# Kernel optimization log

Measured on AMD Instinct MI355X. Metric: run time of the kernel, lower is better.

Reference implementation:

```python
import jax, jax.numpy as jnp
import numpy as np

N_NODES = 50000
N_EDGES = 600000
D = 128
LN_EPS = 1e-5


def setup_inputs() -> dict:
    key = jax.random.key(0)
    ks = jax.random.split(key, 10)
    s = 1.0 / np.sqrt(D)
    return {
        "node_reps": jax.random.normal(ks[0], (N_NODES, D), jnp.float32),
        "edge_reps": jax.random.normal(ks[1], (N_EDGES, D), jnp.float32),
        "src_idx": jax.random.randint(ks[2], (N_EDGES,), 0, N_NODES, jnp.int32),
        "dst_idx": jnp.sort(jax.random.randint(ks[3], (N_EDGES,), 0, N_NODES, jnp.int32)),
        "Wq": jax.random.normal(ks[4], (D, D), jnp.float32) * s,
        "Wk": jax.random.normal(ks[5], (D, D), jnp.float32) * s,
        "Wv": jax.random.normal(ks[6], (D, D), jnp.float32) * s,
        "Wo": jax.random.normal(ks[7], (D, D), jnp.float32) * s,
        "ln_gamma": jnp.ones((D,), jnp.float32),
        "ln_beta": jnp.zeros((D,), jnp.float32),
        "W1": jax.random.normal(ks[8], (3 * D, D), jnp.float32) * (1.0 / np.sqrt(3 * D)),
        "b1": jnp.zeros((D,), jnp.float32),
        "W2": jax.random.normal(ks[9], (D, D), jnp.float32) * s,
        "b2": jnp.zeros((D,), jnp.float32),
    }


def _layer_norm(x, g, b):
    mu = jnp.mean(x, axis=-1, keepdims=True)
    var = jnp.mean(jnp.square(x - mu), axis=-1, keepdims=True)
    return (x - mu) * jax.lax.rsqrt(var + LN_EPS) * g + b


def reference(node_reps, edge_reps, src_idx, dst_idx, Wq, Wk, Wv, Wo,
              ln_gamma, ln_beta, W1, b1, W2, b2):
    n_nodes, d = node_reps.shape
    # dense projections once per node (kernel-friendly GEMMs)
    q = node_reps @ Wq                                  # [N, d]
    k_nodes = node_reps @ Wk                            # [N, d]
    v_nodes = node_reps @ Wv                            # [N, d]
    # per-edge gather + edge bias
    k_e = k_nodes[src_idx] + edge_reps                  # [E, d]
    scores = jnp.sum(q[dst_idx] * k_e, axis=-1) / jnp.sqrt(jnp.float32(d))  # [E]
    # segment softmax over edges sharing the same dst node
    seg_max = jax.ops.segment_max(scores, dst_idx, num_segments=n_nodes)
    ex = jnp.exp(scores - seg_max[dst_idx])
    denom = jax.ops.segment_sum(ex, dst_idx, num_segments=n_nodes)
    alpha = ex / denom[dst_idx]                          # [E]
    v_e = v_nodes[src_idx] + edge_reps                   # [E, d]
    agg = jax.ops.segment_sum(alpha[:, None] * v_e, dst_idx, num_segments=n_nodes)  # [N, d]
    updated = _layer_norm(node_reps + agg @ Wo, ln_gamma, ln_beta)  # [N, d]
    # triplet fusion MLP over (dst node, edge, src node)
    h_trip = jnp.concatenate([node_reps[dst_idx], edge_reps, node_reps[src_idx]], axis=-1)  # [E, 3d]
    fused = jax.nn.relu(h_trip @ W1 + b1) @ W2 + b2      # [E, d]
    return updated, fused
```

## Files before the change

kernel.cpp:

```cpp
#include <hip/hip_runtime.h>
#include <hip/hip_bf16.h>

#define NN 50000
#define NE 600000
#define D 128

typedef __bf16 bf16x8 __attribute__((ext_vector_type(8)));
typedef __bf16 bf16x4 __attribute__((ext_vector_type(4)));
typedef float f32x4 __attribute__((ext_vector_type(4)));


static __device__ __forceinline__ bf16x8 load_a_frag_nc(const float* __restrict__ A,
                                                        int row, int k0) {
  const f32x4* p = (const f32x4*)(A + (size_t)row * D + k0);
  f32x4 v0 = p[0], v1 = p[1];
  bf16x8 r;
  r[0] = (__bf16)v0[0]; r[1] = (__bf16)v0[1]; r[2] = (__bf16)v0[2]; r[3] = (__bf16)v0[3];
  r[4] = (__bf16)v1[0]; r[5] = (__bf16)v1[1]; r[6] = (__bf16)v1[2]; r[7] = (__bf16)v1[3];
  return r;
}

static __device__ __forceinline__ void stage_a_tile128(const float* __restrict__ A, int M,
                                                       int row_base, char* lds, int tid) {
  const int l32 = tid & 31;
  const int g = tid >> 5;
#pragma unroll
  for (int it = 0; it < 16; ++it) {
    int rl = it * 8 + g;
    int r = row_base + rl;
    f32x4 v = {};
    if (r < M) v = *(const f32x4*)(A + (size_t)r * D + l32 * 4);
    bf16x4 b;
    b[0] = (__bf16)v[0]; b[1] = (__bf16)v[1]; b[2] = (__bf16)v[2]; b[3] = (__bf16)v[3];
    int byte = (rl * 256 + l32 * 8) ^ ((rl & 7) << 4);
    *(bf16x4*)(lds + byte) = b;
  }
}

static __device__ __forceinline__ bf16x8 read_a_frag(const char* lds, int rl, int k0) {
  int byte = (rl * 256 + k0 * 2) ^ ((rl & 7) << 4);
  return *(const bf16x8*)(lds + byte);
}

template <int CTRL>
static __device__ __forceinline__ float dpp_add(float x) {
  int v = __builtin_amdgcn_update_dpp(0, __float_as_int(x), CTRL, 0xf, 0xf, true);
  return x + __int_as_float(v);
}

static __device__ __forceinline__ float red32(float x) {
  x = dpp_add<0xB1>(x);
  x = dpp_add<0x4E>(x);
  x = dpp_add<0x124>(x);
  x = dpp_add<0x128>(x);
  return x + __shfl_xor(x, 16, 64);
}

#define CATT 0.12751744612764933f

struct PrepArgs {
  const float* W[8];
  __bf16* WT[8];
  const int* dst;
  int* offs;
};

__global__ void prep_all(PrepArgs pa) {
  int b = blockIdx.x;
  if (b < 512) {
    int w = b >> 6;
    int t = (b & 63) * 256 + threadIdx.x;
    int n = t & 127, k = t >> 7;
    float v = pa.W[w][k * 128 + n];
    if (w == 0) v *= CATT;
    pa.WT[w][n * 128 + k] = (__bf16)v;
  } else {
    int n = (b - 512) * 256 + threadIdx.x;
    if (n > NN) return;
    int lo = 0, hi = NE;
    while (lo < hi) {
      int mid = (lo + hi) >> 1;
      if (pa.dst[mid] < n) lo = mid + 1; else hi = mid;
    }
    pa.offs[n] = lo;
  }
}

struct GemmBatch {
  const __bf16* BT[5];
  void* C[5];
  const float* bias[5];
  int mode[5];
};

__global__ __launch_bounds__(256) void gemm_k128_b(const float* __restrict__ A,
                                                   GemmBatch gb, int M) {
  __shared__ __align__(16) char atile[128 * 256];
  const int y = blockIdx.y;
  const __bf16* __restrict__ BT = gb.BT[y];
  const int tid = threadIdx.x;
  const int lane = tid & 63;
  const int wave = tid >> 6;
  const int wr = wave >> 1, wc = wave & 1;
  const int row0 = blockIdx.x * 128;
  const int col0 = wc * 64;
  const int lr = lane & 15;
  const int lk = (lane >> 4) << 3;

  stage_a_tile128(A, M, row0, atile, tid);
  __syncthreads();

  f32x4 acc[4][4] = {};
#pragma unroll
  for (int kk = 0; kk < 4; ++kk) {
    const int k0 = kk * 32 + lk;
    bf16x8 a[4], b[4];
#pragma unroll
    for (int m = 0; m < 4; ++m) a[m] = read_a_frag(atile, wr * 64 + m * 16 + lr, k0);
#pragma unroll
    for (int n = 0; n < 4; ++n) b[n] = *(const bf16x8*)(BT + (size_t)(col0 + n * 16 + lr) * D + k0);
#pragma unroll
    for (int m = 0; m < 4; ++m)
#pragma unroll
      for (int n = 0; n < 4; ++n)
        acc[m][n] = __builtin_amdgcn_mfma_f32_16x16x32_bf16(a[m], b[n], acc[m][n], 0, 0, 0);
  }
  const int rr = (lane >> 4) * 4;
  float bv[4] = {0.f, 0.f, 0.f, 0.f};
  if (gb.bias[y]) {
#pragma unroll
    for (int n = 0; n < 4; ++n) bv[n] = gb.bias[y][col0 + n * 16 + lr];
  }
  const int mode = gb.mode[y];
#pragma unroll
  for (int m = 0; m < 4; ++m)
#pragma unroll
    for (int j = 0; j < 4; ++j) {
      const int row = row0 + wr * 64 + m * 16 + rr + j;
      if (row < M) {
#pragma unroll
        for (int n = 0; n < 4; ++n) {
          const int c = col0 + n * 16 + lr;
          const float val = acc[m][n][j] + bv[n];
          if (mode == 0) {
            ((float*)gb.C[y])[(size_t)row * D + c] = val;
          } else if (mode == 1) {
            ((__bf16*)gb.C[y])[(size_t)row * D + c] = (__bf16)val;
          } else {
            const int e = ((c >> 2) << 3) + (c & 3) + (mode == 3 ? 4 : 0);
            ((__bf16*)gb.C[y])[(size_t)row * 256 + e] = (__bf16)val;
          }
        }
      }
    }
}

#define LD1(P, K, J, SV)                                                     \
  do {                                                                       \
    const int jj_ = (J);                                                     \
    const int jc_ = jj_ < jm ? jj_ : 0;                                      \
    int si_ = __shfl((SV), jj_ & 31, 32);                                    \
    si_ = jj_ < jm ? si_ : 0;                                                \
    kv##P[K] = *(const bf16x8*)(KV + (size_t)si_ * 256 + (l32 << 3));        \
    ee##P[K] = *(const f32x4*)(edge + (size_t)(s0 + jc_) * D + (l32 << 2));  \
  } while (0)

#define LOADC(P, C)                                                          \
  do {                                                                       \
    const int c4_ = (C) * 4;                                                 \
    const int sv_ = (c4_ < 32) ? sidx0 : sidx1;                              \
    LD1(P, 0, c4_ + 0, sv_); LD1(P, 1, c4_ + 1, sv_);                        \
    LD1(P, 2, c4_ + 2, sv_); LD1(P, 3, c4_ + 3, sv_);                        \
  } while (0)

#define CP1(P, K, J)                                                         \
  do {                                                                       \
    const int jj_ = (J);                                                     \
    f32x4 ef_ = ee##P[K];                                                    \
    float x0_ = (float)kv##P[K][0] + ef_[0];                                 \
    float x1_ = (float)kv##P[K][1] + ef_[1];                                 \
    float x2_ = (float)kv##P[K][2] + ef_[2];                                 \
    float x3_ = (float)kv##P[K][3] + ef_[3];                                 \
    float pp_ = fmaf(qs[1], x1_, qs[0] * x0_) + fmaf(qs[3], x3_, qs[2] * x2_); \
    float s_ = red32(pp_);                                                   \
    float w_ = jj_ < jm ? exp2f(s_) : 0.f;                                   \
    l += w_;                                                                 \
    a[0] = fmaf(w_, (float)kv##P[K][4] + ef_[0], a[0]);                      \
    a[1] = fmaf(w_, (float)kv##P[K][5] + ef_[1], a[1]);                      \
    a[2] = fmaf(w_, (float)kv##P[K][6] + ef_[2], a[2]);                      \
    a[3] = fmaf(w_, (float)kv##P[K][7] + ef_[3], a[3]);                      \
  } while (0)

#define COMPC(P, C)                                                          \
  do {                                                                       \
    const int cc4_ = (C) * 4;                                                \
    CP1(P, 0, cc4_ + 0); CP1(P, 1, cc4_ + 1);                                \
    CP1(P, 2, cc4_ + 2); CP1(P, 3, cc4_ + 3);                                \
  } while (0)

#define MEMFENCE asm volatile("" ::: "memory")

__global__ __launch_bounds__(256) __attribute__((amdgpu_waves_per_eu(4)))
void fused_edge_attn(
    const float* __restrict__ edge,
    const __bf16* __restrict__ W1bT,
    const __bf16* __restrict__ W2T,
    const __bf16* __restrict__ P1,
    const __bf16* __restrict__ P3,
    const int* __restrict__ dst,
    const int* __restrict__ src,
    const float* __restrict__ b2,
    float* __restrict__ out_fused,
    const float* __restrict__ Q,
    const __bf16* __restrict__ KV,
    const int* __restrict__ offs,
    const __bf16* __restrict__ WoT,
    const float* __restrict__ noderep,
    const float* __restrict__ gamma,
    const float* __restrict__ beta,
    float* __restrict__ out_updated) {
  __shared__ __align__(16) char buf[64 * 256];
  const int tid = threadIdx.x;
  const int b = blockIdx.x;
  const int x = b & 7;
  const int t = b >> 3;
  const int grp = (t / 5) * 8 + x;
  const int role = t % 5;
  if (grp >= 3125) return;

  if (role >= 2) {
    const int ebi = grp * 3 + (role - 2);
    const int eb = ebi * 64;
    const int lane = tid & 63;
    const int wave = tid >> 6;
    const int wr = wave >> 1, wc = wave & 1;
    const int lr = lane & 15;
    const int lk = (lane >> 4) << 3;
    const int col0 = wc * 64;
    const int rr = (lane >> 4) * 4;

    f32x4 acc[2][4] = {};
#pragma unroll
    for (int kk = 0; kk < 4; ++kk) {
      const int k0 = kk * 32 + lk;
      bf16x8 a[2], bm[4];
#pragma unroll
      for (int m = 0; m < 2; ++m) a[m] = load_a_frag_nc(edge, eb + wr * 32 + m * 16 + lr, k0);
#pragma unroll
      for (int n = 0; n < 4; ++n) bm[n] = *(const bf16x8*)(W1bT + (size_t)(col0 + n * 16 + lr) * D + k0);
#pragma unroll
      for (int m = 0; m < 2; ++m)
#pragma unroll
        for (int n = 0; n < 4; ++n)
          acc[m][n] = __builtin_amdgcn_mfma_f32_16x16x32_bf16(a[m], bm[n], acc[m][n], 0, 0, 0);
    }

#pragma unroll
    for (int m = 0; m < 2; ++m) {
#pragma unroll
      for (int j = 0; j < 4; ++j) {
        const int rl = wr * 32 + m * 16 + rr + j;
        const __bf16* __restrict__ p1r = P1 + (size_t)dst[eb + rl] * D;
        const __bf16* __restrict__ p3r = P3 + (size_t)src[eb + rl] * D;
#pragma unroll
        for (int n = 0; n < 4; ++n) {
          const int c = col0 + n * 16 + lr;
          float v = fmaxf(acc[m][n][j] + (float)p1r[c] + (float)p3r[c], 0.f);
          int byte = (rl * 256 + c * 2) ^ ((rl & 7) << 4);
          *(__bf16*)(buf + byte) = (__bf16)v;
        }
      }
    }
    __syncthreads();

    float b2v[4];
#pragma unroll
    for (int n = 0; n < 4; ++n) b2v[n] = b2[col0 + n * 16 + lr];
    f32x4 acc2[2][4] = {};
#pragma unroll
    for (int kk = 0; kk < 4; ++kk) {
      const int k0 = kk * 32 + lk;
      bf16x8 a[2], bm[4];
#pragma unroll
      for (int m = 0; m < 2; ++m) a[m] = read_a_frag(buf, wr * 32 + m * 16 + lr, k0);
#pragma unroll
      for (int n = 0; n < 4; ++n) bm[n] = *(const bf16x8*)(W2T + (size_t)(col0 + n * 16 + lr) * D + k0);
#pragma unroll
      for (int m = 0; m < 2; ++m)
#pragma unroll
        for (int n = 0; n < 4; ++n)
          acc2[m][n] = __builtin_amdgcn_mfma_f32_16x16x32_bf16(a[m], bm[n], acc2[m][n], 0, 0, 0);
    }
#pragma unroll
    for (int m = 0; m < 2; ++m)
#pragma unroll
      for (int j = 0; j < 4; ++j) {
        int rl = wr * 32 + m * 16 + rr + j;
        int e = eb + rl;
#pragma unroll
        for (int n = 0; n < 4; ++n) {
          int c = col0 + n * 16 + lr;
          out_fused[(size_t)e * D + c] = acc2[m][n][j] + b2v[n];
        }
      }
  } else {
    const int nw = tid >> 5;
    const int node = (grp * 2 + role) * 8 + nw;
    const int l32 = tid & 31;
    int s0 = offs[node], s1 = offs[node + 1];
    int cnt = s1 - s0;
    f32x4 qs = *(const f32x4*)(Q + (size_t)node * D + l32 * 4);
    float l = 0.f;
    f32x4 a = {0.f, 0.f, 0.f, 0.f};

    const int jm = cnt < 64 ? cnt : 64;
    if (jm > 0) {
      int sidx0 = 0, sidx1 = 0;
      if (l32 < cnt) sidx0 = src[s0 + l32];
      if (l32 + 32 < cnt) sidx1 = src[s0 + 32 + l32];
      bf16x8 kv0[4], kv1[4];
      f32x4 ee0[4], ee1[4];
      const int nch = (jm + 3) >> 2;
      LOADC(0, 0);
      MEMFENCE;
      for (int c = 0; c < nch; c += 2) {
        if (c + 1 < nch) LOADC(1, c + 1);
        MEMFENCE;
        COMPC(0, c);
        if (c + 2 < nch) LOADC(0, c + 2);
        MEMFENCE;
        if (c + 1 < nch) COMPC(1, c + 1);
      }
      for (int i = 64; i < cnt; ++i) {
        int si = src[s0 + i];
        bf16x8 kvx = *(const bf16x8*)(KV + (size_t)si * 256 + (l32 << 3));
        f32x4 ef = *(const f32x4*)(edge + (size_t)(s0 + i) * D + (l32 << 2));
        float x0 = (float)kvx[0] + ef[0], x1 = (float)kvx[1] + ef[1];
        float x2 = (float)kvx[2] + ef[2], x3 = (float)kvx[3] + ef[3];
        float pp = fmaf(qs[1], x1, qs[0] * x0) + fmaf(qs[3], x3, qs[2] * x2);
        float w = exp2f(red32(pp));
        l += w;
        a[0] = fmaf(w, (float)kvx[4] + ef[0], a[0]);
        a[1] = fmaf(w, (float)kvx[5] + ef[1], a[1]);
        a[2] = fmaf(w, (float)kvx[6] + ef[2], a[2]);
        a[3] = fmaf(w, (float)kvx[7] + ef[3], a[3]);
      }
    }
    float inv = l > 0.f ? 1.f / l : 0.f;
    f32x4 r;
    r[0] = a[0] * inv; r[1] = a[1] * inv; r[2] = a[2] * inv; r[3] = a[3] * inv;

    {
      bf16x4 rb;
      rb[0] = (__bf16)r[0]; rb[1] = (__bf16)r[1];
      rb[2] = (__bf16)r[2]; rb[3] = (__bf16)r[3];
      int byte = (nw * 256 + l32 * 8) ^ ((nw & 7) << 4);
      *(bf16x4*)(buf + byte) = rb;
    }
    __syncthreads();

    {
      const int wave = tid >> 6;
      const int lane = tid & 63;
      const int lr = lane & 15;
      const int lk = (lane >> 4) << 3;
      f32x4 acc[2] = {};
#pragma unroll
      for (int kk = 0; kk < 4; ++kk) {
        int k0 = kk * 32 + lk;
        bf16x8 af = read_a_frag(buf, lr, k0);
#pragma unroll
        for (int tt = 0; tt < 2; ++tt) {
          int nn = wave * 2 + tt;
          bf16x8 bm = *(const bf16x8*)(WoT + (size_t)(nn * 16 + lr) * D + k0);
          acc[tt] = __builtin_amdgcn_mfma_f32_16x16x32_bf16(af, bm, acc[tt], 0, 0, 0);
        }
      }
      float* xl = (float*)(buf + 8192);
      const int rr = (lane >> 4) * 4;
      if (rr < 8) {
#pragma unroll
        for (int tt = 0; tt < 2; ++tt) {
          int nn = wave * 2 + tt;
#pragma unroll
          for (int j = 0; j < 4; ++j)
            xl[(rr + j) * 128 + nn * 16 + lr] = acc[tt][j];
        }
      }
    }
    __syncthreads();

    {
      const float* xl = (const float*)(buf + 8192);
      f32x4 xv = *(const f32x4*)(xl + nw * 128 + l32 * 4);
      f32x4 nv = *(const f32x4*)(noderep + (size_t)node * D + l32 * 4);
      float x0 = xv[0] + nv[0], x1 = xv[1] + nv[1];
      float x2 = xv[2] + nv[2], x3 = xv[3] + nv[3];
      float s = red32(x0 + x1 + x2 + x3);
      float mu = s * (1.f / 128.f);
      float d0 = x0 - mu, d1 = x1 - mu, d2 = x2 - mu, d3 = x3 - mu;
      float vv = red32(d0 * d0 + d1 * d1 + d2 * d2 + d3 * d3);
      float rstd = rsqrtf(vv * (1.f / 128.f) + 1e-5f);
      f32x4 g = *(const f32x4*)(gamma + l32 * 4);
      f32x4 bb = *(const f32x4*)(beta + l32 * 4);
      f32x4 o;
      o[0] = d0 * rstd * g[0] + bb[0];
      o[1] = d1 * rstd * g[1] + bb[1];
      o[2] = d2 * rstd * g[2] + bb[2];
      o[3] = d3 * rstd * g[3] + bb[3];
      *(f32x4*)(out_updated + (size_t)node * D + l32 * 4) = o;
    }
  }
}

extern "C" void kernel_launch(void* const* d_in, const int* in_sizes, int n_in,
                              void* d_out, int out_size, void* d_ws, size_t ws_size,
                              hipStream_t stream) {
  const float* node = (const float*)d_in[0];
  const float* edge = (const float*)d_in[1];
  const int* src = (const int*)d_in[2];
  const int* dst = (const int*)d_in[3];
  const float* Wq = (const float*)d_in[4];
  const float* Wk = (const float*)d_in[5];
  const float* Wv = (const float*)d_in[6];
  const float* Wo = (const float*)d_in[7];
  const float* gamma = (const float*)d_in[8];
  const float* beta = (const float*)d_in[9];
  const float* W1 = (const float*)d_in[10];
  const float* b1 = (const float*)d_in[11];
  const float* W2 = (const float*)d_in[12];
  const float* b2 = (const float*)d_in[13];

  float* out_updated = (float*)d_out;
  float* out_fused = (float*)d_out + (size_t)NN * D;

  char* ws = (char*)d_ws;
  size_t o = 0;
  auto take = [&](size_t bytes) {
    char* p = ws + o;
    o = (o + bytes + 255) & ~(size_t)255;
    return p;
  };
  int* offs = (int*)take((NN + 1) * sizeof(int));
  __bf16* WqT = (__bf16*)take(128 * 128 * 2);
  __bf16* WkT = (__bf16*)take(128 * 128 * 2);
  __bf16* WvT = (__bf16*)take(128 * 128 * 2);
  __bf16* WoT = (__bf16*)take(128 * 128 * 2);
  __bf16* W1aT = (__bf16*)take(128 * 128 * 2);
  __bf16* W1bT = (__bf16*)take(128 * 128 * 2);
  __bf16* W1cT = (__bf16*)take(128 * 128 * 2);
  __bf16* W2T = (__bf16*)take(128 * 128 * 2);
  float* Qb = (float*)take((size_t)NN * D * 4);
  __bf16* KVb = (__bf16*)take((size_t)NN * 256 * 2);
  __bf16* P1b = (__bf16*)take((size_t)NN * D * 2);
  __bf16* P3b = (__bf16*)take((size_t)NN * D * 2);

  PrepArgs pa;
  pa.W[0] = Wq; pa.WT[0] = WqT;
  pa.W[1] = Wk; pa.WT[1] = WkT;
  pa.W[2] = Wv; pa.WT[2] = WvT;
  pa.W[3] = Wo; pa.WT[3] = WoT;
  pa.W[4] = W1; pa.WT[4] = W1aT;
  pa.W[5] = W1 + 128 * 128; pa.WT[5] = W1bT;
  pa.W[6] = W1 + 256 * 128; pa.WT[6] = W1cT;
  pa.W[7] = W2; pa.WT[7] = W2T;
  pa.dst = dst; pa.offs = offs;
  prep_all<<<512 + (NN + 256) / 256, 256, 0, stream>>>(pa);

  int gnode = (NN + 127) / 128;
  GemmBatch gb;
  gb.BT[0] = WqT;  gb.C[0] = Qb;  gb.bias[0] = nullptr; gb.mode[0] = 0;
  gb.BT[1] = WkT;  gb.C[1] = KVb; gb.bias[1] = nullptr; gb.mode[1] = 2;
  gb.BT[2] = WvT;  gb.C[2] = KVb; gb.bias[2] = nullptr; gb.mode[2] = 3;
  gb.BT[3] = W1aT; gb.C[3] = P1b; gb.bias[3] = b1;      gb.mode[3] = 1;
  gb.BT[4] = W1cT; gb.C[4] = P3b; gb.bias[4] = nullptr; gb.mode[4] = 1;
  gemm_k128_b<<<dim3(gnode, 5), 256, 0, stream>>>(node, gb, NN);

  fused_edge_attn<<<15640, 256, 0, stream>>>(edge, W1bT, W2T, P1b, P3b, dst, src,
                                             b2, out_fused, Qb, KVb, offs,
                                             WoT, node, gamma, beta, out_updated);
}
```

Baseline: 433.9 us.

## Split fused role-based edge/attention kernel into separate edge MLP and attention kernels

The single kernel that interleaved edge-MLP blocks and node-attention blocks by role is split into two launches: edge_mlp with 64-edge tiles and attn_node with 8 nodes per block. The attention kernel gets a smaller LDS footprint, a waves_per_eu hint of 3 instead of 4, and loses the compiler memory fences between load and compute chunks. The aim is to let each kernel use resources suited to its own work instead of sharing one register/LDS budget. The cost is that the two workloads no longer overlap within one grid, and there is an extra launch.

```diff
diff --git a/kernel.cpp b/kernel.cpp
--- a/kernel.cpp
+++ b/kernel.cpp
@@ -8,6 +8,8 @@
 typedef __bf16 bf16x8 __attribute__((ext_vector_type(8)));
 typedef __bf16 bf16x4 __attribute__((ext_vector_type(4)));
 typedef float f32x4 __attribute__((ext_vector_type(4)));
+
+#define MFMA(a, b, c) __builtin_amdgcn_mfma_f32_16x16x32_bf16((a), (b), (c), 0, 0, 0)
 
 
 static __device__ __forceinline__ bf16x8 load_a_frag_nc(const float* __restrict__ A,
@@ -123,7 +125,7 @@
     for (int m = 0; m < 4; ++m)
 #pragma unroll
       for (int n = 0; n < 4; ++n)
-        acc[m][n] = __builtin_amdgcn_mfma_f32_16x16x32_bf16(a[m], b[n], acc[m][n], 0, 0, 0);
+        acc[m][n] = MFMA(a[m], b[n], acc[m][n]);
   }
   const int rr = (lane >> 4) * 4;
   float bv[4] = {0.f, 0.f, 0.f, 0.f};
@@ -151,6 +153,93 @@
             ((__bf16*)gb.C[y])[(size_t)row * 256 + e] = (__bf16)val;
           }
         }
+      }
+    }
+}
+
+__global__ __launch_bounds__(256) void edge_mlp(
+    const float* __restrict__ edge,
+    const __bf16* __restrict__ W1bT,
+    const __bf16* __restrict__ W2T,
+    const __bf16* __restrict__ P1,
+    const __bf16* __restrict__ P3,
+    const int* __restrict__ dst,
+    const int* __restrict__ src,
+    const float* __restrict__ b2,
+    float* __restrict__ out_fused) {
+  __shared__ __align__(16) char buf[64 * 256];
+  const int tid = threadIdx.x;
+  const int eb = blockIdx.x * 64;
+  const int lane = tid & 63;
+  const int wave = tid >> 6;
+  const int wr = wave >> 1, wc = wave & 1;
+  const int lr = lane & 15;
+  const int lk = (lane >> 4) << 3;
+  const int col0 = wc * 64;
+  const int rr = (lane >> 4) * 4;
+
+  f32x4 acc[2][4] = {};
+#pragma unroll
+  for (int kk = 0; kk < 4; ++kk) {
+    const int k0 = kk * 32 + lk;
+    bf16x8 a[2], bm[4];
+#pragma unroll
+    for (int m = 0; m < 2; ++m) a[m] = load_a_frag_nc(edge, eb + wr * 32 + m * 16 + lr, k0);
+#pragma unroll
+    for (int n = 0; n < 4; ++n) bm[n] = *(const bf16x8*)(W1bT + (size_t)(col0 + n * 16 + lr) * D + k0);
+#pragma unroll
+    for (int m = 0; m < 2; ++m)
+#pragma unroll
+      for (int n = 0; n < 4; ++n)
+        acc[m][n] = MFMA(a[m], bm[n], acc[m][n]);
+  }
+
+#pragma unroll
+  for (int m = 0; m < 2; ++m) {
+#pragma unroll
+    for (int j = 0; j < 4; ++j) {
+      const int rl = wr * 32 + m * 16 + rr + j;
+      const __bf16* __restrict__ p1r = P1 + (size_t)dst[eb + rl] * D;
+      const __bf16* __restrict__ p3r = P3 + (size_t)src[eb + rl] * D;
+#pragma unroll
+      for (int n = 0; n < 4; ++n) {
+        const int c = col0 + n * 16 + lr;
+        float v = fmaxf(acc[m][n][j] + (float)p1r[c] + (float)p3r[c], 0.f);
+        int byte = (rl * 256 + c * 2) ^ ((rl & 7) << 4);
+        *(__bf16*)(buf + byte) = (__bf16)v;
+      }
+    }
+  }
+  __syncthreads();
+
+  float b2v[4];
+#pragma unroll
+  for (int n = 0; n < 4; ++n) b2v[n] = b2[col0 + n * 16 + lr];
+  f32x4 acc2[2][4] = {};
+#pragma unroll
+  for (int kk = 0; kk < 4; ++kk) {
+    const int k0 = kk * 32 + lk;
+    bf16x8 a[2], bm[4];
+#pragma unroll
+    for (int m = 0; m < 2; ++m) a[m] = read_a_frag(buf, wr * 32 + m * 16 + lr, k0);
+#pragma unroll
+    for (int n = 0; n < 4; ++n) bm[n] = *(const bf16x8*)(W2T + (size_t)(col0 + n * 16 + lr) * D + k0);
+#pragma unroll
+    for (int m = 0; m < 2; ++m)
+#pragma unroll
+      for (int n = 0; n < 4; ++n)
+        acc2[m][n] = MFMA(a[m], bm[n], acc2[m][n]);
+  }
+#pragma unroll
+  for (int m = 0; m < 2; ++m)
+#pragma unroll
+    for (int j = 0; j < 4; ++j) {
+      int rl = wr * 32 + m * 16 + rr + j;
+      int e = eb + rl;
+#pragma unroll
+      for (int n = 0; n < 4; ++n) {
+        int c = col0 + n * 16 + lr;
+        out_fused[(size_t)e * D + c] = acc2[m][n][j] + b2v[n];
       }
     }
 }
@@ -198,19 +287,10 @@
     CP1(P, 2, cc4_ + 2); CP1(P, 3, cc4_ + 3);                                \
   } while (0)
 
-#define MEMFENCE asm volatile("" ::: "memory")
-
-__global__ __launch_bounds__(256) __attribute__((amdgpu_waves_per_eu(4)))
-void fused_edge_attn(
+__global__ __launch_bounds__(256) __attribute__((amdgpu_waves_per_eu(3)))
+void attn_node(
     const float* __restrict__ edge,
-    const __bf16* __restrict__ W1bT,
-    const __bf16* __restrict__ W2T,
-    const __bf16* __restrict__ P1,
-    const __bf16* __restrict__ P3,
-    const int* __restrict__ dst,
     const int* __restrict__ src,
-    const float* __restrict__ b2,
-    float* __restrict__ out_fused,
     const float* __restrict__ Q,
     const __bf16* __restrict__ KV,
     const int* __restrict__ offs,
@@ -219,197 +299,110 @@
     const float* __restrict__ gamma,
     const float* __restrict__ beta,
     float* __restrict__ out_updated) {
-  __shared__ __align__(16) char buf[64 * 256];
+  __shared__ __align__(16) char buf[8192];
   const int tid = threadIdx.x;
-  const int b = blockIdx.x;
-  const int x = b & 7;
-  const int t = b >> 3;
-  const int grp = (t / 5) * 8 + x;
-  const int role = t % 5;
-  if (grp >= 3125) return;
-
-  if (role >= 2) {
-    const int ebi = grp * 3 + (role - 2);
-    const int eb = ebi * 64;
+  const int nw = tid >> 5;
+  const int node = blockIdx.x * 8 + nw;
+  const int l32 = tid & 31;
+  int s0 = offs[node], s1 = offs[node + 1];
+  int cnt = s1 - s0;
+  f32x4 qs = *(const f32x4*)(Q + (size_t)node * D + l32 * 4);
+  float l = 0.f;
+  f32x4 a = {0.f, 0.f, 0.f, 0.f};
+
+  const int jm = cnt < 64 ? cnt : 64;
+  if (jm > 0) {
+    int sidx0 = 0, sidx1 = 0;
+    if (l32 < cnt) sidx0 = src[s0 + l32];
+    if (l32 + 32 < cnt) sidx1 = src[s0 + 32 + l32];
+    bf16x8 kv0[4], kv1[4];
+    f32x4 ee0[4], ee1[4];
+    const int nch = (jm + 3) >> 2;
+    LOADC(0, 0);
+    for (int c = 0; c < nch; c += 2) {
+      if (c + 1 < nch) LOADC(1, c + 1);
+      COMPC(0, c);
+      if (c + 2 < nch) LOADC(0, c + 2);
+      if (c + 1 < nch) COMPC(1, c + 1);
+    }
+    for (int i = 64; i < cnt; ++i) {
+      int si = src[s0 + i];
+      bf16x8 kvx = *(const bf16x8*)(KV + (size_t)si * 256 + (l32 << 3));
+      f32x4 ef = *(const f32x4*)(edge + (size_t)(s0 + i) * D + (l32 << 2));
+      float x0 = (float)kvx[0] + ef[0], x1 = (float)kvx[1] + ef[1];
+      float x2 = (float)kvx[2] + ef[2], x3 = (float)kvx[3] + ef[3];
+      float pp = fmaf(qs[1], x1, qs[0] * x0) + fmaf(qs[3], x3, qs[2] * x2);
+      float w = exp2f(red32(pp));
+      l += w;
+      a[0] = fmaf(w, (float)kvx[4] + ef[0], a[0]);
+      a[1] = fmaf(w, (float)kvx[5] + ef[1], a[1]);
+      a[2] = fmaf(w, (float)kvx[6] + ef[2], a[2]);
+      a[3] = fmaf(w, (float)kvx[7] + ef[3], a[3]);
+    }
+  }
+  float inv = l > 0.f ? 1.f / l : 0.f;
+  f32x4 r;
+  r[0] = a[0] * inv; r[1] = a[1] * inv; r[2] = a[2] * inv; r[3] = a[3] * inv;
+
+  {
+    bf16x4 rb;
+    rb[0] = (__bf16)r[0]; rb[1] = (__bf16)r[1];
+    rb[2] = (__bf16)r[2]; rb[3] = (__bf16)r[3];
+    int byte = (nw * 256 + l32 * 8) ^ ((nw & 7) << 4);
+    *(bf16x4*)(buf + byte) = rb;
+  }
+  __syncthreads();
+
+  {
+    const int wave = tid >> 6;
     const int lane = tid & 63;
-    const int wave = tid >> 6;
-    const int wr = wave >> 1, wc = wave & 1;
     const int lr = lane & 15;
     const int lk = (lane >> 4) << 3;
-    const int col0 = wc * 64;
+    f32x4 acc[2] = {};
+#pragma unroll
+    for (int kk = 0; kk < 4; ++kk) {
+      int k0 = kk * 32 + lk;
+      bf16x8 af = read_a_frag(buf, lr, k0);
+#pragma unroll
+      for (int tt = 0; tt < 2; ++tt) {
+        int nn = wave * 2 + tt;
+        bf16x8 bm = *(const bf16x8*)(WoT + (size_t)(nn * 16 + lr) * D + k0);
+        acc[tt] = MFMA(af, bm, acc[tt]);
+      }
+    }
+    float* xl = (float*)(buf + 4096);
     const int rr = (lane >> 4) * 4;
-
-    f32x4 acc[2][4] = {};
-#pragma unroll
-    for (int kk = 0; kk < 4; ++kk) {
-      const int k0 = kk * 32 + lk;
-      bf16x8 a[2], bm[4];
-#pragma unroll
-      for (int m = 0; m < 2; ++m) a[m] = load_a_frag_nc(edge, eb + wr * 32 + m * 16 + lr, k0);
-#pragma unroll
-      for (int n = 0; n < 4; ++n) bm[n] = *(const bf16x8*)(W1bT + (size_t)(col0 + n * 16 + lr) * D + k0);
-#pragma unroll
-      for (int m = 0; m < 2; ++m)
-#pragma unroll
-        for (int n = 0; n < 4; ++n)
-          acc[m][n] = __builtin_amdgcn_mfma_f32_16x16x32_bf16(a[m], bm[n], acc[m][n], 0, 0, 0);
-    }
-
-#pragma unroll
-    for (int m = 0; m < 2; ++m) {
-#pragma unroll
-      for (int j = 0; j < 4; ++j) {
-        const int rl = wr * 32 + m * 16 + rr + j;
-        const __bf16* __restrict__ p1r = P1 + (size_t)dst[eb + rl] * D;
-        const __bf16* __restrict__ p3r = P3 + (size_t)src[eb + rl] * D;
-#pragma unroll
-        for (int n = 0; n < 4; ++n) {
-          const int c = col0 + n * 16 + lr;
-          float v = fmaxf(acc[m][n][j] + (float)p1r[c] + (float)p3r[c], 0.f);
-          int byte = (rl * 256 + c * 2) ^ ((rl & 7) << 4);
-          *(__bf16*)(buf + byte) = (__bf16)v;
-        }
+    if (rr < 8) {
+#pragma unroll
+      for (int tt = 0; tt < 2; ++tt) {
+        int nn = wave * 2 + tt;
+#pragma unroll
+        for (int j = 0; j < 4; ++j)
+          xl[(rr + j) * 128 + nn * 16 + lr] = acc[tt][j];
       }
     }
-    __syncthreads();
-
-    float b2v[4];
-#pragma unroll
-    for (int n = 0; n < 4; ++n) b2v[n] = b2[col0 + n * 16 + lr];
-    f32x4 acc2[2][4] = {};
-#pragma unroll
-    for (int kk = 0; kk < 4; ++kk) {
-      const int k0 = kk * 32 + lk;
-      bf16x8 a[2], bm[4];
-#pragma unroll
-      for (int m = 0; m < 2; ++m) a[m] = read_a_frag(buf, wr * 32 + m * 16 + lr, k0);
-#pragma unroll
-      for (int n = 0; n < 4; ++n) bm[n] = *(const bf16x8*)(W2T + (size_t)(col0 + n * 16 + lr) * D + k0);
-#pragma unroll
-      for (int m = 0; m < 2; ++m)
-#pragma unroll
-        for (int n = 0; n < 4; ++n)
-          acc2[m][n] = __builtin_amdgcn_mfma_f32_16x16x32_bf16(a[m], bm[n], acc2[m][n], 0, 0, 0);
-    }
-#pragma unroll
-    for (int m = 0; m < 2; ++m)
-#pragma unroll
-      for (int j = 0; j < 4; ++j) {
-        int rl = wr * 32 + m * 16 + rr + j;
-        int e = eb + rl;
-#pragma unroll
-        for (int n = 0; n < 4; ++n) {
-          int c = col0 + n * 16 + lr;
-          out_fused[(size_t)e * D + c] = acc2[m][n][j] + b2v[n];
-        }
-      }
-  } else {
-    const int nw = tid >> 5;
-    const int node = (grp * 2 + role) * 8 + nw;
-    const int l32 = tid & 31;
-    int s0 = offs[node], s1 = offs[node + 1];
-    int cnt = s1 - s0;
-    f32x4 qs = *(const f32x4*)(Q + (size_t)node * D + l32 * 4);
-    float l = 0.f;
-    f32x4 a = {0.f, 0.f, 0.f, 0.f};
-
-    const int jm = cnt < 64 ? cnt : 64;
-    if (jm > 0) {
-      int sidx0 = 0, sidx1 = 0;
-      if (l32 < cnt) sidx0 = src[s0 + l32];
-      if (l32 + 32 < cnt) sidx1 = src[s0 + 32 + l32];
-      bf16x8 kv0[4], kv1[4];
-      f32x4 ee0[4], ee1[4];
-      const int nch = (jm + 3) >> 2;
-      LOADC(0, 0);
-      MEMFENCE;
-      for (int c = 0; c < nch; c += 2) {
-        if (c + 1 < nch) LOADC(1, c + 1);
-        MEMFENCE;
-        COMPC(0, c);
-        if (c + 2 < nch) LOADC(0, c + 2);
-        MEMFENCE;
-        if (c + 1 < nch) COMPC(1, c + 1);
-      }
-      for (int i = 64; i < cnt; ++i) {
-        int si = src[s0 + i];
-        bf16x8 kvx = *(const bf16x8*)(KV + (size_t)si * 256 + (l32 << 3));
-        f32x4 ef = *(const f32x4*)(edge + (size_t)(s0 + i) * D + (l32 << 2));
-        float x0 = (float)kvx[0] + ef[0], x1 = (float)kvx[1] + ef[1];
-        float x2 = (float)kvx[2] + ef[2], x3 = (float)kvx[3] + ef[3];
-        float pp = fmaf(qs[1], x1, qs[0] * x0) + fmaf(qs[3], x3, qs[2] * x2);
-        float w = exp2f(red32(pp));
-        l += w;
-        a[0] = fmaf(w, (float)kvx[4] + ef[0], a[0]);
-        a[1] = fmaf(w, (float)kvx[5] + ef[1], a[1]);
-        a[2] = fmaf(w, (float)kvx[6] + ef[2], a[2]);
-        a[3] = fmaf(w, (float)kvx[7] + ef[3], a[3]);
-      }
-    }
-    float inv = l > 0.f ? 1.f / l : 0.f;
-    f32x4 r;
-    r[0] = a[0] * inv; r[1] = a[1] * inv; r[2] = a[2] * inv; r[3] = a[3] * inv;
-
-    {
-      bf16x4 rb;
-      rb[0] = (__bf16)r[0]; rb[1] = (__bf16)r[1];
-      rb[2] = (__bf16)r[2]; rb[3] = (__bf16)r[3];
-      int byte = (nw * 256 + l32 * 8) ^ ((nw & 7) << 4);
-      *(bf16x4*)(buf + byte) = rb;
-    }
-    __syncthreads();
-
-    {
-      const int wave = tid >> 6;
-      const int lane = tid & 63;
-      const int lr = lane & 15;
-      const int lk = (lane >> 4) << 3;
-      f32x4 acc[2] = {};
-#pragma unroll
-      for (int kk = 0; kk < 4; ++kk) {
-        int k0 = kk * 32 + lk;
-        bf16x8 af = read_a_frag(buf, lr, k0);
-#pragma unroll
-        for (int tt = 0; tt < 2; ++tt) {
-          int nn = wave * 2 + tt;
-          bf16x8 bm = *(const bf16x8*)(WoT + (size_t)(nn * 16 + lr) * D + k0);
-          acc[tt] = __builtin_amdgcn_mfma_f32_16x16x32_bf16(af, bm, acc[tt], 0, 0, 0);
-        }
-      }
-      float* xl = (float*)(buf + 8192);
-      const int rr = (lane >> 4) * 4;
-      if (rr < 8) {
-#pragma unroll
-        for (int tt = 0; tt < 2; ++tt) {
-          int nn = wave * 2 + tt;
-#pragma unroll
-          for (int j = 0; j < 4; ++j)
-            xl[(rr + j) * 128 + nn * 16 + lr] = acc[tt][j];
-        }
-      }
-    }
-    __syncthreads();
-
-    {
-      const float* xl = (const float*)(buf + 8192);
-      f32x4 xv = *(const f32x4*)(xl + nw * 128 + l32 * 4);
-      f32x4 nv = *(const f32x4*)(noderep + (size_t)node * D + l32 * 4);
-      float x0 = xv[0] + nv[0], x1 = xv[1] + nv[1];
-      float x2 = xv[2] + nv[2], x3 = xv[3] + nv[3];
-      float s = red32(x0 + x1 + x2 + x3);
-      float mu = s * (1.f / 128.f);
-      float d0 = x0 - mu, d1 = x1 - mu, d2 = x2 - mu, d3 = x3 - mu;
-      float vv = red32(d0 * d0 + d1 * d1 + d2 * d2 + d3 * d3);
-      float rstd = rsqrtf(vv * (1.f / 128.f) + 1e-5f);
-      f32x4 g = *(const f32x4*)(gamma + l32 * 4);
-      f32x4 bb = *(const f32x4*)(beta + l32 * 4);
-      f32x4 o;
-      o[0] = d0 * rstd * g[0] + bb[0];
-      o[1] = d1 * rstd * g[1] + bb[1];
-      o[2] = d2 * rstd * g[2] + bb[2];
-      o[3] = d3 * rstd * g[3] + bb[3];
-      *(f32x4*)(out_updated + (size_t)node * D + l32 * 4) = o;
-    }
+  }
+  __syncthreads();
+
+  {
+    const float* xl = (const float*)(buf + 4096);
+    f32x4 xv = *(const f32x4*)(xl + nw * 128 + l32 * 4);
+    f32x4 nv = *(const f32x4*)(noderep + (size_t)node * D + l32 * 4);
+    float x0 = xv[0] + nv[0], x1 = xv[1] + nv[1];
+    float x2 = xv[2] + nv[2], x3 = xv[3] + nv[3];
+    float s = red32(x0 + x1 + x2 + x3);
+    float mu = s * (1.f / 128.f);
+    float d0 = x0 - mu, d1 = x1 - mu, d2 = x2 - mu, d3 = x3 - mu;
+    float vv = red32(d0 * d0 + d1 * d1 + d2 * d2 + d3 * d3);
+    float rstd = rsqrtf(vv * (1.f / 128.f) + 1e-5f);
+    f32x4 g = *(const f32x4*)(gamma + l32 * 4);
+    f32x4 bb = *(const f32x4*)(beta + l32 * 4);
+    f32x4 o;
+    o[0] = d0 * rstd * g[0] + bb[0];
+    o[1] = d1 * rstd * g[1] + bb[1];
+    o[2] = d2 * rstd * g[2] + bb[2];
+    o[3] = d3 * rstd * g[3] + bb[3];
+    *(f32x4*)(out_updated + (size_t)node * D + l32 * 4) = o;
   }
 }
 
@@ -476,7 +469,8 @@
   gb.BT[4] = W1cT; gb.C[4] = P3b; gb.bias[4] = nullptr; gb.mode[4] = 1;
   gemm_k128_b<<<dim3(gnode, 5), 256, 0, stream>>>(node, gb, NN);
 
-  fused_edge_attn<<<15640, 256, 0, stream>>>(edge, W1bT, W2T, P1b, P3b, dst, src,
-                                             b2, out_fused, Qb, KVb, offs,
-                                             WoT, node, gamma, beta, out_updated);
-}
+  edge_mlp<<<NE / 64, 256, 0, stream>>>(edge, W1bT, W2T, P1b, P3b, dst, src,
+                                        b2, out_fused);
+  attn_node<<<NN / 8, 256, 0, stream>>>(edge, src, Qb, KVb, offs,
+                                        WoT, node, gamma, beta, out_updated);
+}
```

After: 471.1 us. 8.6% more time.
